# Optimization experiments

Measured on AMD Instinct MI355X. Metric: run time of the kernel, lower is better.

The kernel has to match this reference:

```python
import math
import jax, jax.numpy as jnp
import numpy as np

B, S, D, H, L, V, W, FF = 2, 1024, 512, 8, 6, 32000, 64, 2048
HD = D // H
PAD = 0


def setup_inputs() -> dict:
    key = jax.random.key(0)
    ks = jax.random.split(key, 8)
    init = lambda k, shape: jax.random.normal(k, shape, jnp.float32) * 0.02
    # avoid pad_token_id=0 so no row of the attention mask is fully masked (torch would NaN there too)
    input_ids = jax.random.randint(ks[0], (B, S), 1, V)
    return dict(
        input_ids=input_ids,
        emb=init(ks[1], (V, D)),
        Wqkv=init(ks[2], (L, 3 * D, D)), bqkv=jnp.zeros((L, 3 * D), jnp.float32),
        Wo=init(ks[3], (L, D, D)), bo=jnp.zeros((L, D), jnp.float32),
        W1=init(ks[4], (L, 2 * FF, D)), b1=jnp.zeros((L, 2 * FF), jnp.float32),
        W2=init(ks[5], (L, D, FF)), b2=jnp.zeros((L, D), jnp.float32),
        ln1_g=jnp.ones((L, D), jnp.float32), ln1_b=jnp.zeros((L, D), jnp.float32),
        ln2_g=jnp.ones((L, D), jnp.float32), ln2_b=jnp.zeros((L, D), jnp.float32),
        lnf_g=jnp.ones((D,), jnp.float32), lnf_b=jnp.zeros((D,), jnp.float32),
    )


def _ln(x, g, b, eps=1e-5):
    m = x.mean(-1, keepdims=True)
    v = x.var(-1, keepdims=True)  # biased, matches torch LayerNorm
    return (x - m) / jnp.sqrt(v + eps) * g + b


def _pos_enc(seq_len, d_model):
    pos = jnp.arange(seq_len, dtype=jnp.float32)[:, None]
    div = jnp.exp(jnp.arange(0, d_model, 2, dtype=jnp.float32) * (-math.log(10000.0) / d_model))
    pe = jnp.zeros((seq_len, d_model), jnp.float32)
    pe = pe.at[:, 0::2].set(jnp.sin(pos * div))
    pe = pe.at[:, 1::2].set(jnp.cos(pos * div))
    return pe


def _forward(input_ids, emb, Wqkv, bqkv, Wo, bo, W1, b1, W2, b2,
             ln1_g, ln1_b, ln2_g, ln2_b, lnf_g, lnf_b):
    NEG = jnp.finfo(jnp.float32).min
    idx = jnp.arange(S)
    rel = idx[:, None] - idx[None, :]                      # [S,S], i - j
    win = (jnp.arange(H) + 1) * W                          # per-head window sizes
    valid = (rel[None] >= 0) & (rel[None] < win[:, None, None])  # [H,S,S]
    not_pad = input_ids != PAD                             # [B,S] key padding
    vis = valid[None, :, :, :] & not_pad[:, None, None, :] # [B,H,S,S]
    mask = jnp.where(vis, 0.0, NEG).astype(jnp.float32)

    x = emb[input_ids] + _pos_enc(S, D)                    # [B,S,D]
    for l in range(L):
        # self-attention (torch nn.MultiheadAttention, batch_first)
        qkv = x @ Wqkv[l].T + bqkv[l]                      # [B,S,3D]
        q, k, v = jnp.split(qkv, 3, axis=-1)
        q = q.reshape(B, S, H, HD).transpose(0, 2, 1, 3)
        k = k.reshape(B, S, H, HD).transpose(0, 2, 1, 3)
        v = v.reshape(B, S, H, HD).transpose(0, 2, 1, 3)
        scores = jnp.einsum('bhqd,bhkd->bhqk', q, k) / math.sqrt(HD) + mask
        p = jax.nn.softmax(scores, axis=-1)
        a = jnp.einsum('bhqk,bhkd->bhqd', p, v).transpose(0, 2, 1, 3).reshape(B, S, D)
        a = a @ Wo[l].T + bo[l]
        x = _ln(x + a, ln1_g[l], ln1_b[l])
        # SwiGLU-style FFN: linear1 -> chunk -> a * silu(b) -> linear2
        h = x @ W1[l].T + b1[l]
        u, g = jnp.split(h, 2, axis=-1)
        ff = (u * jax.nn.silu(g)) @ W2[l].T + b2[l]
        x = _ln(x + ff, ln2_g[l], ln2_b[l])
    x = _ln(x, lnf_g, lnf_b)
    return x @ emb.T                                       # tied lm_head, no bias


def reference(input_ids, emb, Wqkv, bqkv, Wo, bo, W1, b1, W2, b2,
              ln1_g, ln1_b, ln2_g, ln2_b, lnf_g, lnf_b):
    return _forward(input_ids, emb, Wqkv, bqkv, Wo, bo, W1, b1, W2, b2,
                    ln1_g, ln1_b, ln2_g, ln2_b, lnf_g, lnf_b)
```

## Files before the change

### kernel.cpp

```cpp
#include <hip/hip_runtime.h>

#define SEQ    1024
#define DIM    512
#define NHEAD  8
#define NLAYER 6
#define FFDIM  2048
#define HDIM   64
#define BATCH  2
#define VOCAB  32000
#define ROWS   (BATCH * SEQ)

typedef __attribute__((ext_vector_type(8))) __bf16 bf16x8;
typedef __attribute__((ext_vector_type(4))) float  f32x4;

__device__ __forceinline__ unsigned short f2bf(float f) {
    unsigned int u = __float_as_uint(f);
    u += 0x7FFFu + ((u >> 16) & 1u);
    return (unsigned short)(u >> 16);
}
__device__ __forceinline__ float bf2f(unsigned short u) {
    return __uint_as_float(((unsigned int)u) << 16);
}
__device__ __forceinline__ float lo_f(unsigned int u) { return __uint_as_float(u << 16); }
__device__ __forceinline__ float hi_f(unsigned int u) { return __uint_as_float(u & 0xFFFF0000u); }
__device__ __forceinline__ unsigned int pack2(float a, float b) {
    return (unsigned int)f2bf(a) | ((unsigned int)f2bf(b) << 16);
}

__global__ __launch_bounds__(256) void cvt_kernel(const float* __restrict__ in,
                                                  unsigned short* __restrict__ out) {
    int base = (blockIdx.x * 256 + threadIdx.x) * 8;
    float4 a = *(const float4*)(in + base);
    float4 b = *(const float4*)(in + base + 4);
    *(uint4*)(out + base) = make_uint4(pack2(a.x, a.y), pack2(a.z, a.w),
                                       pack2(b.x, b.y), pack2(b.z, b.w));
}

__global__ __launch_bounds__(256) void embed_kernel(const int* __restrict__ ids,
                                                    const float* __restrict__ emb,
                                                    unsigned short* __restrict__ x) {
    int t8   = blockIdx.x * 256 + threadIdx.x;
    int base = t8 * 8;
    int row  = base >> 9;
    int d0   = base & (DIM - 1);
    int s    = row & (SEQ - 1);
    int id   = ids[row];
    const float* er = emb + (size_t)id * DIM + d0;
    float4 ea = *(const float4*)(er);
    float4 eb = *(const float4*)(er + 4);
    float e[8] = {ea.x, ea.y, ea.z, ea.w, eb.x, eb.y, eb.z, eb.w};
    unsigned int ou[4];
#pragma unroll
    for (int m = 0; m < 4; ++m) {
        int de = d0 + 2 * m;
        float div = expf((float)de * -0.017988946039015984f);
        float arg = (float)s * div;
        ou[m] = pack2(e[2 * m] + sinf(arg), e[2 * m + 1] + cosf(arg));
    }
    *(uint4*)(x + base) = make_uint4(ou[0], ou[1], ou[2], ou[3]);
}

template <int MODE>
__global__ __launch_bounds__(256) void gemm_kernel(const unsigned short* __restrict__ A,
                                                   const unsigned short* __restrict__ W,
                                                   const float* __restrict__ bias,
                                                   void* __restrict__ Cout,
                                                   int M, int N, int K,
                                                   unsigned short* __restrict__ vT) {
    __shared__ __align__(16) unsigned short As[128 * 64];
    __shared__ __align__(16) unsigned short Bs[128 * 64];
    const int tid  = threadIdx.x;
    const int nwg = (int)(gridDim.x * gridDim.y);
    const int bid = (int)(blockIdx.y * gridDim.x + blockIdx.x);
    const int cpx = nwg >> 3;
    const int wk  = (bid & 7) * cpx + (bid >> 3);
    const int m0  = (wk & 15) * 128;
    const int n0  = (wk >> 4) * 128;
    const int lane = tid & 63;
    const int wv   = tid >> 6;
    const int wr   = wv >> 1, wc = wv & 1;
    const int frow = lane & 15, quad = lane >> 4;

    f32x4 acc[4][4] = {};

    const int srow = wv * 32 + (lane >> 3);
    const int scol = (lane & 7) * 8;
    const unsigned short* Ag = A + (size_t)(m0 + srow) * K + scol;
    const unsigned short* Wg = W + (size_t)(n0 + srow) * K + scol;
    unsigned short* Asw = &As[(wv * 32) * 64];
    unsigned short* Bsw = &Bs[(wv * 32) * 64];

    for (int k0 = 0; k0 < K; k0 += 64) {
#pragma unroll
        for (int p = 0; p < 4; ++p) {
            __builtin_amdgcn_global_load_lds(
                (const __attribute__((address_space(1))) void*)(Ag + (size_t)(p * 8) * K + k0),
                (__attribute__((address_space(3))) void*)(Asw + p * 8 * 64), 16, 0, 0);
            __builtin_amdgcn_global_load_lds(
                (const __attribute__((address_space(1))) void*)(Wg + (size_t)(p * 8) * K + k0),
                (__attribute__((address_space(3))) void*)(Bsw + p * 8 * 64), 16, 0, 0);
        }
        __syncthreads();
#pragma unroll
        for (int kk = 0; kk < 64; kk += 32) {
            bf16x8 af[4], bfr[4];
#pragma unroll
            for (int t = 0; t < 4; ++t) {
                af[t]  = *(const bf16x8*)&As[(wr * 64 + t * 16 + frow) * 64 + kk + quad * 8];
                bfr[t] = *(const bf16x8*)&Bs[(wc * 64 + t * 16 + frow) * 64 + kk + quad * 8];
            }
#pragma unroll
            for (int am = 0; am < 4; ++am)
#pragma unroll
                for (int bn = 0; bn < 4; ++bn)
                    acc[am][bn] = __builtin_amdgcn_mfma_f32_16x16x32_bf16(af[am], bfr[bn], acc[am][bn], 0, 0, 0);
        }
        __syncthreads();
    }

#pragma unroll
    for (int am = 0; am < 4; ++am) {
#pragma unroll
        for (int bn = 0; bn < 4; ++bn) {
            int col  = n0 + wc * 64 + bn * 16 + frow;
            float bv = bias ? bias[col] : 0.0f;
            int rowb = m0 + wr * 64 + am * 16 + quad * 4;
            if (MODE == 2 && col >= 1024) {
                float v0 = acc[am][bn][0] + bv;
                float v1 = acc[am][bn][1] + bv;
                float v2 = acc[am][bn][2] + bv;
                float v3 = acc[am][bn][3] + bv;
                *(uint2*)&vT[(size_t)(col - 1024) * ROWS + rowb] =
                    make_uint2(pack2(v0, v1), pack2(v2, v3));
            } else {
#pragma unroll
                for (int r = 0; r < 4; ++r) {
                    int row = rowb + r;
                    float v = acc[am][bn][r] + bv;
                    if (MODE == 1)      ((float*)Cout)[(size_t)row * N + col] = v;
                    else if (MODE == 2) ((unsigned short*)Cout)[(size_t)row * 1024 + col] = f2bf(v);
                    else                ((unsigned short*)Cout)[(size_t)row * N + col] = f2bf(v);
                }
            }
        }
    }
}

__global__ __launch_bounds__(512) void attn_kernel(const unsigned short* __restrict__ qk,
                                                   const unsigned short* __restrict__ vT,
                                                   unsigned short* __restrict__ out) {
    __shared__ __align__(16) unsigned short P_lds[8][16 * 40];
    const int tid  = threadIdx.x;
    const int w    = tid >> 6, lane = tid & 63;
    const int c    = lane & 15, g = lane >> 4;
    const int b    = blockIdx.x >> 6;
    const int qt   = blockIdx.x & 63;
    const int h    = w;
    const int qbase = qt * 16;
    const int win   = (h + 1) * 64;
    const int qmax  = qbase + 15;
    int kbs = qbase - win + 1; if (kbs < 0) kbs = 0; kbs &= ~31;

    const size_t tok0 = (size_t)b * SEQ;

    const unsigned short* qp = qk + (tok0 + qbase + c) * 1024 + h * HDIM + g * 8;
    const bf16x8 qf0 = *(const bf16x8*)qp;
    const bf16x8 qf1 = *(const bf16x8*)(qp + 32);

    f32x4 o[4] = {};
    float m[4]    = {-3.0e38f, -3.0e38f, -3.0e38f, -3.0e38f};
    float lsum[4] = {};

    unsigned short* pl = P_lds[w];

    for (int kb = kbs; kb <= qmax; kb += 32) {
        f32x4 s[2] = {};
#pragma unroll
        for (int st = 0; st < 2; ++st) {
            const unsigned short* kp = qk + (tok0 + kb + st * 16 + c) * 1024 + DIM + h * HDIM + g * 8;
            bf16x8 kf0 = *(const bf16x8*)kp;
            bf16x8 kf1 = *(const bf16x8*)(kp + 32);
            s[st] = __builtin_amdgcn_mfma_f32_16x16x32_bf16(qf0, kf0, s[st], 0, 0, 0);
            s[st] = __builtin_amdgcn_mfma_f32_16x16x32_bf16(qf1, kf1, s[st], 0, 0, 0);
        }
        float sm[2][4];
        bool  va[2][4];
        float tmax[4];
#pragma unroll
        for (int r = 0; r < 4; ++r) {
            int i  = qbase + 4 * g + r;
            int j0 = kb + c, j1 = j0 + 16;
            bool v0 = (unsigned)(i - j0) < (unsigned)win;
            bool v1 = (unsigned)(i - j1) < (unsigned)win;
            va[0][r] = v0; va[1][r] = v1;
            sm[0][r] = v0 ? s[0][r] * 0.125f : -3.0e38f;
            sm[1][r] = v1 ? s[1][r] * 0.125f : -3.0e38f;
            float t = fmaxf(sm[0][r], sm[1][r]);
#pragma unroll
            for (int off = 1; off < 16; off <<= 1) t = fmaxf(t, __shfl_xor(t, off));
            tmax[r] = t;
        }
#pragma unroll
        for (int r = 0; r < 4; ++r) {
            float mnew = fmaxf(m[r], tmax[r]);
            float scal = __expf(m[r] - mnew);
            float p0 = va[0][r] ? __expf(sm[0][r] - mnew) : 0.0f;
            float p1 = va[1][r] ? __expf(sm[1][r] - mnew) : 0.0f;
            float rs = p0 + p1;
#pragma unroll
            for (int off = 1; off < 16; off <<= 1) rs += __shfl_xor(rs, off);
            lsum[r] = lsum[r] * scal + rs;
            m[r] = mnew;
#pragma unroll
            for (int t = 0; t < 4; ++t) o[t][r] *= scal;
            pl[(4 * g + r) * 40 + c]      = f2bf(p0);
            pl[(4 * g + r) * 40 + c + 16] = f2bf(p1);
        }
        bf16x8 pf = *(const bf16x8*)&pl[c * 40 + g * 8];
#pragma unroll
        for (int t = 0; t < 4; ++t) {
            const unsigned short* vp = vT + (size_t)(h * HDIM + t * 16 + c) * ROWS + tok0 + kb + g * 8;
            bf16x8 vf = *(const bf16x8*)vp;
            o[t] = __builtin_amdgcn_mfma_f32_16x16x32_bf16(pf, vf, o[t], 0, 0, 0);
        }
    }

    float inv[4];
#pragma unroll
    for (int r = 0; r < 4; ++r) inv[r] = 1.0f / lsum[r];
#pragma unroll
    for (int t = 0; t < 4; ++t)
#pragma unroll
        for (int r = 0; r < 4; ++r)
            out[(tok0 + qbase + 4 * g + r) * DIM + h * HDIM + t * 16 + c] = f2bf(o[t][r] * inv[r]);
}

__global__ __launch_bounds__(256) void ln_kernel(const unsigned short* __restrict__ xin,
                                                 const unsigned short* __restrict__ res,
                                                 const float* __restrict__ g,
                                                 const float* __restrict__ bta,
                                                 unsigned short* __restrict__ out) {
    const int tid = threadIdx.x;
    const int w   = tid >> 6, lane = tid & 63;
    const int row = blockIdx.x * 4 + w;
    const int c0  = lane * 8;
    const size_t base = (size_t)row * DIM + c0;

    uint4 xv = *(const uint4*)(xin + base);
    float v[8] = {lo_f(xv.x), hi_f(xv.x), lo_f(xv.y), hi_f(xv.y),
                  lo_f(xv.z), hi_f(xv.z), lo_f(xv.w), hi_f(xv.w)};
    if (res) {
        uint4 rv = *(const uint4*)(res + base);
        v[0] += lo_f(rv.x); v[1] += hi_f(rv.x); v[2] += lo_f(rv.y); v[3] += hi_f(rv.y);
        v[4] += lo_f(rv.z); v[5] += hi_f(rv.z); v[6] += lo_f(rv.w); v[7] += hi_f(rv.w);
    }
    float sum = 0.0f, sq = 0.0f;
#pragma unroll
    for (int t = 0; t < 8; ++t) { sum += v[t]; sq += v[t] * v[t]; }
#pragma unroll
    for (int off = 32; off >= 1; off >>= 1) { sum += __shfl_xor(sum, off); sq += __shfl_xor(sq, off); }
    float mean = sum * (1.0f / DIM);
    float var  = sq * (1.0f / DIM) - mean * mean;
    float rstd = rsqrtf(var + 1e-5f);

    float4 ga = *(const float4*)(g + c0);
    float4 gb = *(const float4*)(g + c0 + 4);
    float4 ba = *(const float4*)(bta + c0);
    float4 bb = *(const float4*)(bta + c0 + 4);
    float gf[8] = {ga.x, ga.y, ga.z, ga.w, gb.x, gb.y, gb.z, gb.w};
    float bf[8] = {ba.x, ba.y, ba.z, ba.w, bb.x, bb.y, bb.z, bb.w};
    unsigned int o[4];
#pragma unroll
    for (int mm = 0; mm < 4; ++mm) {
        float a0 = (v[2 * mm]     - mean) * rstd * gf[2 * mm]     + bf[2 * mm];
        float a1 = (v[2 * mm + 1] - mean) * rstd * gf[2 * mm + 1] + bf[2 * mm + 1];
        o[mm] = pack2(a0, a1);
    }
    *(uint4*)(out + base) = make_uint4(o[0], o[1], o[2], o[3]);
}

__global__ __launch_bounds__(256) void swiglu_kernel(const unsigned short* __restrict__ h,
                                                     unsigned short* __restrict__ o) {
    int t8   = blockIdx.x * 256 + threadIdx.x;
    int base = t8 * 8;
    int r = base >> 11;
    int c = base & (FFDIM - 1);
    const unsigned short* hr = h + (size_t)r * (2 * FFDIM);
    uint4 uv = *(const uint4*)(hr + c);
    uint4 gv = *(const uint4*)(hr + FFDIM + c);
    float u[8] = {lo_f(uv.x), hi_f(uv.x), lo_f(uv.y), hi_f(uv.y),
                  lo_f(uv.z), hi_f(uv.z), lo_f(uv.w), hi_f(uv.w)};
    float gg[8] = {lo_f(gv.x), hi_f(gv.x), lo_f(gv.y), hi_f(gv.y),
                   lo_f(gv.z), hi_f(gv.z), lo_f(gv.w), hi_f(gv.w)};
    unsigned int ov[4];
#pragma unroll
    for (int m = 0; m < 4; ++m) {
        float g0 = gg[2 * m],     s0 = g0 / (1.0f + expf(-g0));
        float g1 = gg[2 * m + 1], s1 = g1 / (1.0f + expf(-g1));
        ov[m] = pack2(u[2 * m] * s0, u[2 * m + 1] * s1);
    }
    *(uint4*)(o + (size_t)r * FFDIM + c) = make_uint4(ov[0], ov[1], ov[2], ov[3]);
}

extern "C" void kernel_launch(void* const* d_in, const int* in_sizes, int n_in,
                              void* d_out, int out_size, void* d_ws, size_t ws_size,
                              hipStream_t stream) {
    const int*   ids  = (const int*)d_in[0];
    const float* emb  = (const float*)d_in[1];
    const float* Wqkv = (const float*)d_in[2];
    const float* bqkv = (const float*)d_in[3];
    const float* Wo   = (const float*)d_in[4];
    const float* bo   = (const float*)d_in[5];
    const float* W1   = (const float*)d_in[6];
    const float* b1   = (const float*)d_in[7];
    const float* W2   = (const float*)d_in[8];
    const float* b2   = (const float*)d_in[9];
    const float* ln1g = (const float*)d_in[10];
    const float* ln1b = (const float*)d_in[11];
    const float* ln2g = (const float*)d_in[12];
    const float* ln2b = (const float*)d_in[13];
    const float* lnfg = (const float*)d_in[14];
    const float* lnfb = (const float*)d_in[15];

    unsigned short* x    = (unsigned short*)d_ws;
    unsigned short* qk   = x    + (size_t)ROWS * DIM;
    unsigned short* vT   = qk   + (size_t)ROWS * 2 * DIM;
    unsigned short* attn = vT   + (size_t)DIM * ROWS;
    unsigned short* proj = attn + (size_t)ROWS * DIM;
    unsigned short* hbuf = proj + (size_t)ROWS * DIM;
    unsigned short* ffin = hbuf + (size_t)ROWS * 2 * FFDIM;
    unsigned short* WqkvB = ffin + (size_t)ROWS * FFDIM;
    unsigned short* WoB   = WqkvB + (size_t)NLAYER * 3 * DIM * DIM;
    unsigned short* W1B   = WoB   + (size_t)NLAYER * DIM * DIM;
    unsigned short* W2B   = W1B   + (size_t)NLAYER * 2 * FFDIM * DIM;
    unsigned short* embB  = W2B   + (size_t)NLAYER * DIM * FFDIM;

    cvt_kernel<<<NLAYER * 3 * DIM * DIM / 2048, 256, 0, stream>>>(Wqkv, WqkvB);
    cvt_kernel<<<NLAYER * DIM * DIM / 2048, 256, 0, stream>>>(Wo, WoB);
    cvt_kernel<<<NLAYER * 2 * FFDIM * DIM / 2048, 256, 0, stream>>>(W1, W1B);
    cvt_kernel<<<NLAYER * DIM * FFDIM / 2048, 256, 0, stream>>>(W2, W2B);
    cvt_kernel<<<VOCAB * DIM / 2048, 256, 0, stream>>>(emb, embB);

    embed_kernel<<<ROWS * DIM / (256 * 8), 256, 0, stream>>>(ids, emb, x);

    for (int l = 0; l < NLAYER; ++l) {
        gemm_kernel<2><<<dim3(16, 12), 256, 0, stream>>>(x, WqkvB + (size_t)l * 3 * DIM * DIM,
                                                         bqkv + l * 3 * DIM, qk, ROWS, 3 * DIM, DIM, vT);
        attn_kernel<<<BATCH * (SEQ / 16), 512, 0, stream>>>(qk, vT, attn);
        gemm_kernel<0><<<dim3(16, 4), 256, 0, stream>>>(attn, WoB + (size_t)l * DIM * DIM,
                                                        bo + l * DIM, proj, ROWS, DIM, DIM, nullptr);
        ln_kernel<<<ROWS / 4, 256, 0, stream>>>(x, proj, ln1g + l * DIM, ln1b + l * DIM, x);
        gemm_kernel<0><<<dim3(16, 32), 256, 0, stream>>>(x, W1B + (size_t)l * 2 * FFDIM * DIM,
                                                         b1 + l * 2 * FFDIM, hbuf, ROWS, 2 * FFDIM, DIM, nullptr);
        swiglu_kernel<<<ROWS * FFDIM / (256 * 8), 256, 0, stream>>>(hbuf, ffin);
        gemm_kernel<0><<<dim3(16, 4), 256, 0, stream>>>(ffin, W2B + (size_t)l * DIM * FFDIM,
                                                        b2 + l * DIM, attn , ROWS, DIM, FFDIM, nullptr);
        ln_kernel<<<ROWS / 4, 256, 0, stream>>>(x, attn, ln2g + l * DIM, ln2b + l * DIM, x);
    }
    ln_kernel<<<ROWS / 4, 256, 0, stream>>>(x, nullptr, lnfg, lnfb, x);
    gemm_kernel<1><<<dim3(16, VOCAB / 128), 256, 0, stream>>>(x, embB, nullptr,
                                                              d_out, ROWS, VOCAB, DIM, nullptr);
}
```

Baseline: 1.352 ms.

## Fuse SwiGLU into W1 GEMM, widen LM-head tiles, swizzle LDS layout

Adds an NT template parameter to the GEMM so one workgroup can compute two 128-column B tiles. The W1 GEMM uses this to load matching u and g weight rows together and apply SwiGLU in the epilogue, which removes the separate swiglu kernel and the round trip through the hbuf intermediate. The LM-head GEMM switches to 256-wide N tiles so each A tile is reused across more columns. An XOR swizzle on the LDS column index is also added to reduce bank conflicts. The cost is a larger accumulator array and more LDS per workgroup, which raises register pressure under launch_bounds(256,2).

Result: faster. 1.190 ms (-12.0%).

```diff
diff --git a/kernel.cpp b/kernel.cpp
--- a/kernel.cpp
+++ b/kernel.cpp
@@ -60,35 +60,34 @@
     *(uint4*)(x + base) = make_uint4(ou[0], ou[1], ou[2], ou[3]);
 }
 
-template <int MODE>
-__global__ __launch_bounds__(256) void gemm_kernel(const unsigned short* __restrict__ A,
-                                                   const unsigned short* __restrict__ W,
-                                                   const float* __restrict__ bias,
-                                                   void* __restrict__ Cout,
-                                                   int M, int N, int K,
-                                                   unsigned short* __restrict__ vT) {
+template <int MODE, int NT>
+__global__ __launch_bounds__(256, 2) void gemm_kernel(const unsigned short* __restrict__ A,
+                                                      const unsigned short* __restrict__ W,
+                                                      const float* __restrict__ bias,
+                                                      void* __restrict__ Cout,
+                                                      int M, int N, int K,
+                                                      unsigned short* __restrict__ vT) {
     __shared__ __align__(16) unsigned short As[128 * 64];
-    __shared__ __align__(16) unsigned short Bs[128 * 64];
+    __shared__ __align__(16) unsigned short Bs[NT * 128 * 64];
     const int tid  = threadIdx.x;
     const int nwg = (int)(gridDim.x * gridDim.y);
     const int bid = (int)(blockIdx.y * gridDim.x + blockIdx.x);
     const int cpx = nwg >> 3;
     const int wk  = (bid & 7) * cpx + (bid >> 3);
     const int m0  = (wk & 15) * 128;
-    const int n0  = (wk >> 4) * 128;
+    const int ct  = wk >> 4;
+    const int n0  = (MODE == 1) ? ct * 256 : ct * 128;
     const int lane = tid & 63;
     const int wv   = tid >> 6;
     const int wr   = wv >> 1, wc = wv & 1;
     const int frow = lane & 15, quad = lane >> 4;
 
-    f32x4 acc[4][4] = {};
-
-    const int srow = wv * 32 + (lane >> 3);
-    const int scol = (lane & 7) * 8;
-    const unsigned short* Ag = A + (size_t)(m0 + srow) * K + scol;
-    const unsigned short* Wg = W + (size_t)(n0 + srow) * K + scol;
+    f32x4 acc[4][4 * NT] = {};
+
+    const int lrow = lane >> 3;
+    const int scol = ((lane & 7) ^ lrow) * 8;
+    const unsigned short* Ag = A + (size_t)(m0 + wv * 32 + lrow) * K + scol;
     unsigned short* Asw = &As[(wv * 32) * 64];
-    unsigned short* Bsw = &Bs[(wv * 32) * 64];
 
     for (int k0 = 0; k0 < K; k0 += 64) {
 #pragma unroll
@@ -96,23 +95,44 @@
             __builtin_amdgcn_global_load_lds(
                 (const __attribute__((address_space(1))) void*)(Ag + (size_t)(p * 8) * K + k0),
                 (__attribute__((address_space(3))) void*)(Asw + p * 8 * 64), 16, 0, 0);
-            __builtin_amdgcn_global_load_lds(
-                (const __attribute__((address_space(1))) void*)(Wg + (size_t)(p * 8) * K + k0),
-                (__attribute__((address_space(3))) void*)(Bsw + p * 8 * 64), 16, 0, 0);
+        }
+        if (NT == 1) {
+            const unsigned short* Wg = W + (size_t)(n0 + wv * 32 + lrow) * K + scol;
+#pragma unroll
+            for (int p = 0; p < 4; ++p) {
+                __builtin_amdgcn_global_load_lds(
+                    (const __attribute__((address_space(1))) void*)(Wg + (size_t)(p * 8) * K + k0),
+                    (__attribute__((address_space(3))) void*)(&Bs[(wv * 32 + p * 8) * 64]), 16, 0, 0);
+            }
+        } else {
+#pragma unroll
+            for (int q = 0; q < 8; ++q) {
+                int rl = wv * 64 + q * 8;
+                int grow = (MODE == 3) ? (n0 + (rl & 127) + (rl >> 7) * FFDIM)
+                                       : (n0 + rl);
+                const unsigned short* src = W + (size_t)(grow + lrow) * K + scol + k0;
+                __builtin_amdgcn_global_load_lds(
+                    (const __attribute__((address_space(1))) void*)src,
+                    (__attribute__((address_space(3))) void*)(&Bs[rl * 64]), 16, 0, 0);
+            }
         }
         __syncthreads();
 #pragma unroll
         for (int kk = 0; kk < 64; kk += 32) {
-            bf16x8 af[4], bfr[4];
-#pragma unroll
-            for (int t = 0; t < 4; ++t) {
-                af[t]  = *(const bf16x8*)&As[(wr * 64 + t * 16 + frow) * 64 + kk + quad * 8];
-                bfr[t] = *(const bf16x8*)&Bs[(wc * 64 + t * 16 + frow) * 64 + kk + quad * 8];
+            const int gsw = ((kk >> 3) + quad) ^ (frow & 7);
+            bf16x8 af[4], bfr[4 * NT];
+#pragma unroll
+            for (int t = 0; t < 4; ++t)
+                af[t] = *(const bf16x8*)&As[(wr * 64 + t * 16 + frow) * 64 + gsw * 8];
+#pragma unroll
+            for (int t = 0; t < 4 * NT; ++t) {
+                int brow = (t >> 2) * 128 + wc * 64 + (t & 3) * 16 + frow;
+                bfr[t] = *(const bf16x8*)&Bs[brow * 64 + gsw * 8];
             }
 #pragma unroll
             for (int am = 0; am < 4; ++am)
 #pragma unroll
-                for (int bn = 0; bn < 4; ++bn)
+                for (int bn = 0; bn < 4 * NT; ++bn)
                     acc[am][bn] = __builtin_amdgcn_mfma_f32_16x16x32_bf16(af[am], bfr[bn], acc[am][bn], 0, 0, 0);
         }
         __syncthreads();
@@ -120,26 +140,41 @@
 
 #pragma unroll
     for (int am = 0; am < 4; ++am) {
-#pragma unroll
-        for (int bn = 0; bn < 4; ++bn) {
-            int col  = n0 + wc * 64 + bn * 16 + frow;
-            float bv = bias ? bias[col] : 0.0f;
-            int rowb = m0 + wr * 64 + am * 16 + quad * 4;
-            if (MODE == 2 && col >= 1024) {
-                float v0 = acc[am][bn][0] + bv;
-                float v1 = acc[am][bn][1] + bv;
-                float v2 = acc[am][bn][2] + bv;
-                float v3 = acc[am][bn][3] + bv;
-                *(uint2*)&vT[(size_t)(col - 1024) * ROWS + rowb] =
-                    make_uint2(pack2(v0, v1), pack2(v2, v3));
-            } else {
+        int rowb = m0 + wr * 64 + am * 16 + quad * 4;
+        if (MODE == 3) {
+#pragma unroll
+            for (int bn = 0; bn < 4; ++bn) {
+                int colL = wc * 64 + bn * 16 + frow;
+                float bu = bias[n0 + colL];
+                float bg = bias[FFDIM + n0 + colL];
 #pragma unroll
                 for (int r = 0; r < 4; ++r) {
-                    int row = rowb + r;
-                    float v = acc[am][bn][r] + bv;
-                    if (MODE == 1)      ((float*)Cout)[(size_t)row * N + col] = v;
-                    else if (MODE == 2) ((unsigned short*)Cout)[(size_t)row * 1024 + col] = f2bf(v);
-                    else                ((unsigned short*)Cout)[(size_t)row * N + col] = f2bf(v);
+                    float u = acc[am][bn][r] + bu;
+                    float g = acc[am][bn + 4][r] + bg;
+                    float s = g / (1.0f + expf(-g));
+                    ((unsigned short*)Cout)[(size_t)(rowb + r) * N + n0 + colL] = f2bf(u * s);
+                }
+            }
+        } else {
+#pragma unroll
+            for (int bn = 0; bn < 4 * NT; ++bn) {
+                int col = n0 + (bn >> 2) * 128 + wc * 64 + (bn & 3) * 16 + frow;
+                float bv = bias ? bias[col] : 0.0f;
+                if (MODE == 2 && col >= 1024) {
+                    float v0 = acc[am][bn][0] + bv;
+                    float v1 = acc[am][bn][1] + bv;
+                    float v2 = acc[am][bn][2] + bv;
+                    float v3 = acc[am][bn][3] + bv;
+                    *(uint2*)&vT[(size_t)(col - 1024) * ROWS + rowb] =
+                        make_uint2(pack2(v0, v1), pack2(v2, v3));
+                } else {
+#pragma unroll
+                    for (int r = 0; r < 4; ++r) {
+                        float v = acc[am][bn][r] + bv;
+                        if (MODE == 1)      ((float*)Cout)[(size_t)(rowb + r) * N + col] = v;
+                        else if (MODE == 2) ((unsigned short*)Cout)[(size_t)(rowb + r) * 1024 + col] = f2bf(v);
+                        else                ((unsigned short*)Cout)[(size_t)(rowb + r) * N + col] = f2bf(v);
+                    }
                 }
             }
         }
@@ -277,29 +312,6 @@
         o[mm] = pack2(a0, a1);
     }
     *(uint4*)(out + base) = make_uint4(o[0], o[1], o[2], o[3]);
-}
-
-__global__ __launch_bounds__(256) void swiglu_kernel(const unsigned short* __restrict__ h,
-                                                     unsigned short* __restrict__ o) {
-    int t8   = blockIdx.x * 256 + threadIdx.x;
-    int base = t8 * 8;
-    int r = base >> 11;
-    int c = base & (FFDIM - 1);
-    const unsigned short* hr = h + (size_t)r * (2 * FFDIM);
-    uint4 uv = *(const uint4*)(hr + c);
-    uint4 gv = *(const uint4*)(hr + FFDIM + c);
-    float u[8] = {lo_f(uv.x), hi_f(uv.x), lo_f(uv.y), hi_f(uv.y),
-                  lo_f(uv.z), hi_f(uv.z), lo_f(uv.w), hi_f(uv.w)};
-    float gg[8] = {lo_f(gv.x), hi_f(gv.x), lo_f(gv.y), hi_f(gv.y),
-                   lo_f(gv.z), hi_f(gv.z), lo_f(gv.w), hi_f(gv.w)};
-    unsigned int ov[4];
-#pragma unroll
-    for (int m = 0; m < 4; ++m) {
-        float g0 = gg[2 * m],     s0 = g0 / (1.0f + expf(-g0));
-        float g1 = gg[2 * m + 1], s1 = g1 / (1.0f + expf(-g1));
-        ov[m] = pack2(u[2 * m] * s0, u[2 * m + 1] * s1);
-    }
-    *(uint4*)(o + (size_t)r * FFDIM + c) = make_uint4(ov[0], ov[1], ov[2], ov[3]);
 }
 
 extern "C" void kernel_launch(void* const* d_in, const int* in_sizes, int n_in,
@@ -327,8 +339,7 @@
     unsigned short* vT   = qk   + (size_t)ROWS * 2 * DIM;
     unsigned short* attn = vT   + (size_t)DIM * ROWS;
     unsigned short* proj = attn + (size_t)ROWS * DIM;
-    unsigned short* hbuf = proj + (size_t)ROWS * DIM;
-    unsigned short* ffin = hbuf + (size_t)ROWS * 2 * FFDIM;
+    unsigned short* ffin = proj + (size_t)ROWS * DIM;
     unsigned short* WqkvB = ffin + (size_t)ROWS * FFDIM;
     unsigned short* WoB   = WqkvB + (size_t)NLAYER * 3 * DIM * DIM;
     unsigned short* W1B   = WoB   + (size_t)NLAYER * DIM * DIM;
@@ -344,20 +355,19 @@
     embed_kernel<<<ROWS * DIM / (256 * 8), 256, 0, stream>>>(ids, emb, x);
 
     for (int l = 0; l < NLAYER; ++l) {
-        gemm_kernel<2><<<dim3(16, 12), 256, 0, stream>>>(x, WqkvB + (size_t)l * 3 * DIM * DIM,
-                                                         bqkv + l * 3 * DIM, qk, ROWS, 3 * DIM, DIM, vT);
+        gemm_kernel<2, 1><<<dim3(16, 12), 256, 0, stream>>>(x, WqkvB + (size_t)l * 3 * DIM * DIM,
+                                                            bqkv + l * 3 * DIM, qk, ROWS, 3 * DIM, DIM, vT);
         attn_kernel<<<BATCH * (SEQ / 16), 512, 0, stream>>>(qk, vT, attn);
-        gemm_kernel<0><<<dim3(16, 4), 256, 0, stream>>>(attn, WoB + (size_t)l * DIM * DIM,
-                                                        bo + l * DIM, proj, ROWS, DIM, DIM, nullptr);
+        gemm_kernel<0, 1><<<dim3(16, 4), 256, 0, stream>>>(attn, WoB + (size_t)l * DIM * DIM,
+                                                           bo + l * DIM, proj, ROWS, DIM, DIM, nullptr);
         ln_kernel<<<ROWS / 4, 256, 0, stream>>>(x, proj, ln1g + l * DIM, ln1b + l * DIM, x);
-        gemm_kernel<0><<<dim3(16, 32), 256, 0, stream>>>(x, W1B + (size_t)l * 2 * FFDIM * DIM,
-                                                         b1 + l * 2 * FFDIM, hbuf, ROWS, 2 * FFDIM, DIM, nullptr);
-        swiglu_kernel<<<ROWS * FFDIM / (256 * 8), 256, 0, stream>>>(hbuf, ffin);
-        gemm_kernel<0><<<dim3(16, 4), 256, 0, stream>>>(ffin, W2B + (size_t)l * DIM * FFDIM,
-                                                        b2 + l * DIM, attn , ROWS, DIM, FFDIM, nullptr);
+        gemm_kernel<3, 2><<<dim3(16, FFDIM / 128), 256, 0, stream>>>(x, W1B + (size_t)l * 2 * FFDIM * DIM,
+                                                                     b1 + l * 2 * FFDIM, ffin, ROWS, FFDIM, DIM, nullptr);
+        gemm_kernel<0, 1><<<dim3(16, 4), 256, 0, stream>>>(ffin, W2B + (size_t)l * DIM * FFDIM,
+                                                           b2 + l * DIM, attn , ROWS, DIM, FFDIM, nullptr);
         ln_kernel<<<ROWS / 4, 256, 0, stream>>>(x, attn, ln2g + l * DIM, ln2b + l * DIM, x);
     }
     ln_kernel<<<ROWS / 4, 256, 0, stream>>>(x, nullptr, lnfg, lnfb, x);
-    gemm_kernel<1><<<dim3(16, VOCAB / 128), 256, 0, stream>>>(x, embB, nullptr,
-                                                              d_out, ROWS, VOCAB, DIM, nullptr);
-}
+    gemm_kernel<1, 2><<<dim3(16, VOCAB / 256), 256, 0, stream>>>(x, embB, nullptr,
+                                                                 d_out, ROWS, VOCAB, DIM, nullptr);
+}
```
